# Kernel tuning notes

Hardware: AMD Instinct MI355X
Metric: run time of the kernel (lower is better)

The kernel has to match this reference:

```python
import jax, jax.numpy as jnp
import numpy as np

PAD = 1  # module padding

def setup_inputs() -> dict:
    key = jax.random.key(0)
    k1, k2 = jax.random.split(key)
    x = jax.random.normal(k1, (1, 256, 512, 512), dtype=jnp.float32)
    # module uses uniform(-xavier, xavier) with xavier = 1/sqrt(kh*kw)
    xavier = 1.0 / np.sqrt(3 * 3)
    weight = jax.random.uniform(k2, (256, 256, 3, 3), dtype=jnp.float32,
                                minval=-xavier, maxval=xavier)
    return {"x": x, "weight": weight}

def reference(x, weight):
    # Stride-1 cross-correlation with zero padding PAD, matching the
    # module's per-pixel slice*kernel sum (batch must be 1 for that code).
    return jax.lax.conv_general_dilated(
        x, weight,
        window_strides=(1, 1),
        padding=[(PAD, PAD), (PAD, PAD)],
        dimension_numbers=("NCHW", "OIHW", "NCHW"),
    )
```

## Files before the change

kernel.cpp:

```cpp
#include <hip/hip_runtime.h>
#include <stdint.h>

typedef __attribute__((ext_vector_type(8))) __bf16 bf16x8;
typedef __attribute__((ext_vector_type(16))) float f32x16;

constexpr int CIN = 256, COUT = 256, HH = 512, WW = 512;
constexpr int BC = 16;
constexpr int NCB = CIN / BC;
constexpr int CPAD = 20;
constexpr int MT = 128;
constexpr int TY = 8, TX = 32;

__device__ __forceinline__ unsigned short f2bf(float f) {
    union { float f; unsigned int u; } v; v.f = f;
    return (unsigned short)((v.u + 0x7fffu + ((v.u >> 16) & 1u)) >> 16);
}

__device__ __forceinline__ bf16x8 ldsfrag(const unsigned short* p) {
    union { unsigned long long u[2]; bf16x8 v; } r;
    r.u[0] = *reinterpret_cast<const unsigned long long*>(p);
    r.u[1] = *reinterpret_cast<const unsigned long long*>(p + 4);
    return r.v;
}

__global__ void wt_transform2(const float* __restrict__ w, unsigned short* __restrict__ wt2) {
    const int cbtap = blockIdx.x;
    const int cb = cbtap / 9, tap = cbtap - cb * 9;
    #pragma unroll 4
    for (int e = threadIdx.x; e < 4096; e += 256) {
        const int k = e >> 4, ci = e & 15;
        wt2[cbtap * 4096 + e] = f2bf(w[(k * CIN + cb * BC + ci) * 9 + tap]);
    }
}

__global__ __launch_bounds__(256)
void x_transform(const float* __restrict__ x, unsigned short* __restrict__ xb) {
    __shared__ unsigned short Xl[64][264];
    const int y  = blockIdx.x >> 3;
    const int x0 = (blockIdx.x & 7) * 64;
    #pragma unroll
    for (int q = threadIdx.x; q < 4096; q += 256) {
        const int c = q >> 4, p4 = (q & 15) << 2;
        const float4 v = *reinterpret_cast<const float4*>(
            x + ((long long)c * HH + y) * WW + x0 + p4);
        Xl[p4 + 0][c] = f2bf(v.x);
        Xl[p4 + 1][c] = f2bf(v.y);
        Xl[p4 + 2][c] = f2bf(v.z);
        Xl[p4 + 3][c] = f2bf(v.w);
    }
    __syncthreads();
    #pragma unroll
    for (int q = threadIdx.x; q < 2048; q += 256) {
        const int cb = q >> 7, rem = q & 127, px = rem >> 1, h = rem & 1;
        const int4 v = *reinterpret_cast<const int4*>(&Xl[px][cb * 16 + h * 8]);
        *reinterpret_cast<int4*>(
            xb + (((long long)cb * HH + y) * WW + x0 + px) * 16 + h * 8) = v;
    }
}

__global__ __launch_bounds__(256, 2)
void conv_mfma2(const unsigned short* __restrict__ xb, const unsigned short* __restrict__ wt2,
                float* __restrict__ out) {
    __shared__ unsigned short Wlds[9][MT][CPAD];
    __shared__ unsigned short Xt[TY + 2][TX + 2][CPAD];

    const int bid = blockIdx.x;
    const int k0 = (bid & 1) * MT;
    const int tile = bid >> 1;
    const int x0 = (tile & 15) * TX;
    const int y0 = (tile >> 4) * TY;

    const int tid = threadIdx.x;
    const int lane = tid & 63;
    const int wave = tid >> 6;
    const int wm = wave & 1;
    const int wn = wave >> 1;
    const int ln31 = lane & 31;
    const int lh8 = (lane >> 5) * 8;

    f32x16 acc[2][4];
    #pragma unroll
    for (int i = 0; i < 2; ++i)
        #pragma unroll
        for (int j = 0; j < 4; ++j)
            #pragma unroll
            for (int r = 0; r < 16; ++r) acc[i][j][r] = 0.f;

    for (int cb = 0; cb < NCB; ++cb) {
        #pragma unroll
        for (int e = tid; e < 9 * 256; e += 256) {
            const int tap = e >> 8;
            const int kk = (e >> 1) & 127;
            const int h = e & 1;
            const int4 v = *reinterpret_cast<const int4*>(
                wt2 + (((cb * 9 + tap) * 256 + k0 + kk) << 4) + h * 8);
            unsigned long long* d = reinterpret_cast<unsigned long long*>(&Wlds[tap][kk][h * 8]);
            const unsigned long long* s2 = reinterpret_cast<const unsigned long long*>(&v);
            d[0] = s2[0]; d[1] = s2[1];
        }

        for (int rr = wave; rr < TY + 2; rr += 4) {
            const int yy = y0 - 1 + rr;
            const bool rowok = ((unsigned)yy < (unsigned)HH);
            const int xi = lane >> 1, h = lane & 1;
            const int gx = x0 - 1 + xi;
            int4 v; v.x = v.y = v.z = v.w = 0;
            if (rowok && (unsigned)gx < (unsigned)WW)
                v = *reinterpret_cast<const int4*>(
                    xb + (((cb * HH + yy) * WW + gx) << 4) + h * 8);
            unsigned long long* d = reinterpret_cast<unsigned long long*>(&Xt[rr][xi][h * 8]);
            const unsigned long long* s2 = reinterpret_cast<const unsigned long long*>(&v);
            d[0] = s2[0]; d[1] = s2[1];
            if (lane < 4) {
                const int xi2 = 32 + (lane >> 1);
                const int gx2 = x0 - 1 + xi2;
                int4 v2; v2.x = v2.y = v2.z = v2.w = 0;
                if (rowok && gx2 < WW)
                    v2 = *reinterpret_cast<const int4*>(
                        xb + (((cb * HH + yy) * WW + gx2) << 4) + h * 8);
                unsigned long long* d2 = reinterpret_cast<unsigned long long*>(&Xt[rr][xi2][h * 8]);
                const unsigned long long* s3 = reinterpret_cast<const unsigned long long*>(&v2);
                d2[0] = s3[0]; d2[1] = s3[1];
            }
        }
        __syncthreads();

        #pragma unroll
        for (int rr = 0; rr < 3; ++rr) {
            #pragma unroll
            for (int s = 0; s < 3; ++s) {
                const int tap = rr * 3 + s;
                const bf16x8 a0 = ldsfrag(&Wlds[tap][wm * 64 + 0 + ln31][lh8]);
                const bf16x8 a1 = ldsfrag(&Wlds[tap][wm * 64 + 32 + ln31][lh8]);
                #pragma unroll
                for (int j = 0; j < 4; ++j) {
                    const bf16x8 b = ldsfrag(&Xt[wn * 4 + j + rr][s + ln31][lh8]);
                    acc[0][j] = __builtin_amdgcn_mfma_f32_32x32x16_bf16(a0, b, acc[0][j], 0, 0, 0);
                    acc[1][j] = __builtin_amdgcn_mfma_f32_32x32x16_bf16(a1, b, acc[1][j], 0, 0, 0);
                }
            }
        }
        __syncthreads();
    }

    #pragma unroll
    for (int i = 0; i < 2; ++i) {
        const int mb = k0 + wm * 64 + i * 32 + (lane >> 5) * 4;
        #pragma unroll
        for (int j = 0; j < 4; ++j) {
            const long long py = y0 + wn * 4 + j;
            const long long px = x0 + ln31;
            #pragma unroll
            for (int r = 0; r < 16; ++r) {
                const int m = mb + (r & 3) + 8 * (r >> 2);
                out[((long long)m * HH + py) * WW + px] = acc[i][j][r];
            }
        }
    }
}

__global__ void wt_transform(const float* __restrict__ w, unsigned short* __restrict__ wt) {
    int idx = blockIdx.x * 256 + threadIdx.x;
    int tap = idx >> 16;
    int rem = idx & 65535;
    int k = rem >> 8, c = rem & 255;
    wt[idx] = f2bf(w[((k << 8) | c) * 9 + tap]);
}

__global__ __launch_bounds__(256, 3)
void conv_mfma(const float* __restrict__ x, const unsigned short* __restrict__ wt,
               float* __restrict__ out) {
    __shared__ unsigned short Wlds[9][MT][CPAD];
    __shared__ unsigned short Xto[4 + 2][TX + 2][CPAD];

    const int bid = blockIdx.x;
    const int k0 = (bid & 1) * MT;
    const int tile = bid >> 1;
    const int x0 = (tile & 15) * TX;
    const int y0 = (tile >> 4) * 4;

    const int tid = threadIdx.x;
    const int lane = tid & 63;
    const int wave = tid >> 6;
    const int wm = wave & 1;
    const int wn = wave >> 1;
    const int ln31 = lane & 31;
    const int lh8 = (lane >> 5) * 8;

    f32x16 acc[2][2];
    #pragma unroll
    for (int i = 0; i < 2; ++i)
        #pragma unroll
        for (int j = 0; j < 2; ++j)
            #pragma unroll
            for (int r = 0; r < 16; ++r) acc[i][j][r] = 0.f;

    for (int cb = 0; cb < CIN / BC; ++cb) {
        const int c0 = cb * BC;
        for (int e = tid; e < 9 * MT; e += 256) {
            const int tap = e >> 7;
            const int k = e & (MT - 1);
            const unsigned long long* src = reinterpret_cast<const unsigned long long*>(
                wt + ((tap * COUT + (k0 + k)) * CIN + c0));
            unsigned long long* dst = reinterpret_cast<unsigned long long*>(&Wlds[tap][k][0]);
            dst[0] = src[0]; dst[1] = src[1]; dst[2] = src[2]; dst[3] = src[3];
        }
        {
            const int rowid = tid >> 5, lx = tid & 31;
            for (int p = rowid; p < 6 * BC; p += 8) {
                const int rr = p >> 4, c = p & 15;
                const int yy = y0 - 1 + rr;
                const bool rowok = ((unsigned)yy < (unsigned)HH);
                const float* xrow = x + (long long)(c0 + c) * (HH * WW) + (long long)yy * WW;
                const int gx = x0 - 1 + lx;
                float v0 = (rowok && (unsigned)gx < (unsigned)WW) ? xrow[gx] : 0.f;
                Xto[rr][lx][c] = f2bf(v0);
                if (lx < 2) {
                    const int gx2 = x0 + 31 + lx;
                    float v1 = (rowok && gx2 < WW) ? xrow[gx2] : 0.f;
                    Xto[rr][32 + lx][c] = f2bf(v1);
                }
            }
        }
        __syncthreads();
        #pragma unroll
        for (int rr = 0; rr < 3; ++rr) {
            #pragma unroll
            for (int s = 0; s < 3; ++s) {
                const int tap = rr * 3 + s;
                bf16x8 a0 = ldsfrag(&Wlds[tap][wm * 64 + 0 + ln31][lh8]);
                bf16x8 a1 = ldsfrag(&Wlds[tap][wm * 64 + 32 + ln31][lh8]);
                bf16x8 b0 = ldsfrag(&Xto[wn * 2 + 0 + rr][s + ln31][lh8]);
                bf16x8 b1 = ldsfrag(&Xto[wn * 2 + 1 + rr][s + ln31][lh8]);
                acc[0][0] = __builtin_amdgcn_mfma_f32_32x32x16_bf16(a0, b0, acc[0][0], 0, 0, 0);
                acc[0][1] = __builtin_amdgcn_mfma_f32_32x32x16_bf16(a0, b1, acc[0][1], 0, 0, 0);
                acc[1][0] = __builtin_amdgcn_mfma_f32_32x32x16_bf16(a1, b0, acc[1][0], 0, 0, 0);
                acc[1][1] = __builtin_amdgcn_mfma_f32_32x32x16_bf16(a1, b1, acc[1][1], 0, 0, 0);
            }
        }
        __syncthreads();
    }

    #pragma unroll
    for (int i = 0; i < 2; ++i) {
        const int mb = k0 + wm * 64 + i * 32 + (lane >> 5) * 4;
        #pragma unroll
        for (int j = 0; j < 2; ++j) {
            const long long py = y0 + wn * 2 + j;
            const long long px = x0 + ln31;
            #pragma unroll
            for (int r = 0; r < 16; ++r) {
                const int m = mb + (r & 3) + 8 * (r >> 2);
                out[((long long)m * HH + py) * WW + px] = acc[i][j][r];
            }
        }
    }
}

__global__ void conv_naive(const float* __restrict__ x, const float* __restrict__ w,
                           float* __restrict__ out) {
    const int k = blockIdx.x;
    const int y = blockIdx.y;
    const int xx = blockIdx.z * 256 + threadIdx.x;
    float a = 0.f;
    for (int c = 0; c < CIN; ++c) {
        const float* wp = w + ((k * CIN + c) * 9);
        const float* xp = x + (long long)c * HH * WW;
        #pragma unroll
        for (int r = 0; r < 3; ++r) {
            const int yy = y + r - 1;
            if ((unsigned)yy >= (unsigned)HH) continue;
            const float* row = xp + (long long)yy * WW;
            #pragma unroll
            for (int s = 0; s < 3; ++s) {
                const int gx = xx + s - 1;
                const float v = ((unsigned)gx < (unsigned)WW) ? row[gx] : 0.f;
                a += wp[r * 3 + s] * v;
            }
        }
    }
    out[((long long)k * HH + y) * WW + xx] = a;
}

extern "C" void kernel_launch(void* const* d_in, const int* in_sizes, int n_in,
                              void* d_out, int out_size, void* d_ws, size_t ws_size,
                              hipStream_t stream) {
    const float* x = (const float*)d_in[0];
    const float* w = (const float*)d_in[1];
    float* out = (float*)d_out;

    const size_t xb_bytes  = (size_t)NCB * HH * WW * BC * sizeof(unsigned short);
    const size_t wt2_bytes = (size_t)144 * 4096 * sizeof(unsigned short);
    const size_t wt_bytes  = (size_t)9 * 256 * 256 * sizeof(unsigned short);

    if (ws_size >= xb_bytes + wt2_bytes) {
        unsigned short* xb  = (unsigned short*)d_ws;
        unsigned short* wt2 = (unsigned short*)d_ws + xb_bytes / sizeof(unsigned short);
        x_transform<<<4096, 256, 0, stream>>>(x, xb);
        wt_transform2<<<144, 256, 0, stream>>>(w, wt2);
        conv_mfma2<<<2048, 256, 0, stream>>>(xb, wt2, out);
    } else if (ws_size >= wt_bytes) {
        unsigned short* wt = (unsigned short*)d_ws;
        wt_transform<<<2304, 256, 0, stream>>>(w, wt);
        conv_mfma<<<4096, 256, 0, stream>>>(x, wt, out);
    } else {
        conv_naive<<<dim3(256, 512, 2), 256, 0, stream>>>(x, w, out);
    }
}
```

Before: 792.4 us.

## Load conv tiles via global_load_lds, drop LDS padding, swizzle blocks, retile x_transform

Replaces the register-staged global-to-LDS copies in the main conv kernel with direct global_load_lds transfers into unpadded 16-element-wide LDS tiles. Out-of-bounds halo pixels are read from a zeroed global buffer. The next channel block's loads are now issued right after the compute with explicit waitcnt and barriers, and block IDs are swizzled so blocks sharing a tile land near each other. It also splits x_transform into smaller per-channel-group blocks and removes the mid-size fallback path. The risk is that dropping the padding brings back LDS bank conflicts on the bf16x8 fragment reads, and loads are still not double-buffered.

```diff
diff --git a/kernel.cpp b/kernel.cpp
--- a/kernel.cpp
+++ b/kernel.cpp
@@ -7,7 +7,6 @@
 constexpr int CIN = 256, COUT = 256, HH = 512, WW = 512;
 constexpr int BC = 16;
 constexpr int NCB = CIN / BC;
-constexpr int CPAD = 20;
 constexpr int MT = 128;
 constexpr int TY = 8, TX = 32;
 
@@ -16,11 +15,12 @@
     return (unsigned short)((v.u + 0x7fffu + ((v.u >> 16) & 1u)) >> 16);
 }
 
-__device__ __forceinline__ bf16x8 ldsfrag(const unsigned short* p) {
-    union { unsigned long long u[2]; bf16x8 v; } r;
-    r.u[0] = *reinterpret_cast<const unsigned long long*>(p);
-    r.u[1] = *reinterpret_cast<const unsigned long long*>(p + 4);
-    return r.v;
+__device__ __align__(256) unsigned short g_zero16[16] = {};
+
+__device__ __forceinline__ void gload16(const void* g, const void* l) {
+    __builtin_amdgcn_global_load_lds(
+        (const __attribute__((address_space(1))) unsigned int*)g,
+        (__attribute__((address_space(3))) unsigned int*)l, 16, 0, 0);
 }
 
 __global__ void wt_transform2(const float* __restrict__ w, unsigned short* __restrict__ wt2) {
@@ -35,38 +35,43 @@
 
 __global__ __launch_bounds__(256)
 void x_transform(const float* __restrict__ x, unsigned short* __restrict__ xb) {
-    __shared__ unsigned short Xl[64][264];
-    const int y  = blockIdx.x >> 3;
-    const int x0 = (blockIdx.x & 7) * 64;
-    #pragma unroll
-    for (int q = threadIdx.x; q < 4096; q += 256) {
-        const int c = q >> 4, p4 = (q & 15) << 2;
+    __shared__ __align__(16) float Xl[16][72];
+    const int b   = blockIdx.x;
+    const int y   = b >> 5;
+    const int xc  = (b >> 2) & 7;
+    const int cbg = b & 3;
+    const int x0  = xc * 64;
+    const int tid = threadIdx.x;
+    const int ci  = tid >> 4, p4 = (tid & 15) << 2;
+    const int px  = tid >> 2, cig = tid & 3;
+    #pragma unroll 1
+    for (int g = 0; g < 4; ++g) {
+        const int cb = cbg * 4 + g;
         const float4 v = *reinterpret_cast<const float4*>(
-            x + ((long long)c * HH + y) * WW + x0 + p4);
-        Xl[p4 + 0][c] = f2bf(v.x);
-        Xl[p4 + 1][c] = f2bf(v.y);
-        Xl[p4 + 2][c] = f2bf(v.z);
-        Xl[p4 + 3][c] = f2bf(v.w);
-    }
-    __syncthreads();
-    #pragma unroll
-    for (int q = threadIdx.x; q < 2048; q += 256) {
-        const int cb = q >> 7, rem = q & 127, px = rem >> 1, h = rem & 1;
-        const int4 v = *reinterpret_cast<const int4*>(&Xl[px][cb * 16 + h * 8]);
-        *reinterpret_cast<int4*>(
-            xb + (((long long)cb * HH + y) * WW + x0 + px) * 16 + h * 8) = v;
+            x + ((long long)(cb * 16 + ci) * HH + y) * WW + x0 + p4);
+        *reinterpret_cast<float4*>(&Xl[ci][p4]) = v;
+        __syncthreads();
+        ushort4 o;
+        o.x = f2bf(Xl[cig * 4 + 0][px]);
+        o.y = f2bf(Xl[cig * 4 + 1][px]);
+        o.z = f2bf(Xl[cig * 4 + 2][px]);
+        o.w = f2bf(Xl[cig * 4 + 3][px]);
+        *reinterpret_cast<ushort4*>(
+            xb + (((long long)cb * HH + y) * WW + x0 + px) * 16 + cig * 4) = o;
+        __syncthreads();
     }
 }
 
 __global__ __launch_bounds__(256, 2)
-void conv_mfma2(const unsigned short* __restrict__ xb, const unsigned short* __restrict__ wt2,
+void conv_mfma3(const unsigned short* __restrict__ xb, const unsigned short* __restrict__ wt2,
                 float* __restrict__ out) {
-    __shared__ unsigned short Wlds[9][MT][CPAD];
-    __shared__ unsigned short Xt[TY + 2][TX + 2][CPAD];
+    __shared__ __align__(16) unsigned short Wl[9][MT][16];
+    __shared__ __align__(16) unsigned short Xs[TY + 2][36][16];
 
     const int bid = blockIdx.x;
-    const int k0 = (bid & 1) * MT;
-    const int tile = bid >> 1;
+    const int swz = ((bid & 7) << 8) | (bid >> 3);
+    const int k0 = (swz & 1) * MT;
+    const int tile = swz >> 1;
     const int x0 = (tile & 15) * TX;
     const int y0 = (tile >> 4) * TY;
 
@@ -86,61 +91,84 @@
             #pragma unroll
             for (int r = 0; r < 16; ++r) acc[i][j][r] = 0.f;
 
+    const unsigned short* wsrc0 = wt2 + (size_t)k0 * 16 + (size_t)tid * 8;
+    unsigned short* wl = ((unsigned short*)Wl) + (tid >> 6) * 512;
+
+    {
+        const unsigned short* wsrc = wsrc0;
+        #pragma unroll
+        for (int i = 0; i < 9; ++i)
+            gload16(wsrc + (size_t)i * 4096, wl + i * 2048);
+        #pragma unroll
+        for (int t = 0; t < 3; ++t) {
+            const int rr = wave + t * 4;
+            if (rr < TY + 2) {
+                const int yy = y0 - 1 + rr;
+                const bool rok = (unsigned)yy < (unsigned)HH;
+                const size_t rowb = ((size_t)0 * HH + (rok ? yy : 0)) * WW;
+                const int gx = x0 - 1 + (lane >> 1);
+                const bool ok = rok && ((unsigned)gx < (unsigned)WW);
+                const unsigned short* gs = ok ? xb + (rowb + gx) * 16 + (lane & 1) * 8 : g_zero16;
+                gload16(gs, &Xs[rr][0][0]);
+                if (lane < 8) {
+                    const int gx2 = x0 + 31 + (lane >> 1);
+                    const bool ok2 = rok && gx2 < WW;
+                    const unsigned short* gs2 = ok2 ? xb + (rowb + gx2) * 16 + (lane & 1) * 8 : g_zero16;
+                    gload16(gs2, &Xs[rr][32][0]);
+                }
+            }
+        }
+        asm volatile("s_waitcnt vmcnt(0)" ::: "memory");
+        __builtin_amdgcn_s_barrier();
+    }
+
     for (int cb = 0; cb < NCB; ++cb) {
         #pragma unroll
-        for (int e = tid; e < 9 * 256; e += 256) {
-            const int tap = e >> 8;
-            const int kk = (e >> 1) & 127;
-            const int h = e & 1;
-            const int4 v = *reinterpret_cast<const int4*>(
-                wt2 + (((cb * 9 + tap) * 256 + k0 + kk) << 4) + h * 8);
-            unsigned long long* d = reinterpret_cast<unsigned long long*>(&Wlds[tap][kk][h * 8]);
-            const unsigned long long* s2 = reinterpret_cast<const unsigned long long*>(&v);
-            d[0] = s2[0]; d[1] = s2[1];
-        }
-
-        for (int rr = wave; rr < TY + 2; rr += 4) {
-            const int yy = y0 - 1 + rr;
-            const bool rowok = ((unsigned)yy < (unsigned)HH);
-            const int xi = lane >> 1, h = lane & 1;
-            const int gx = x0 - 1 + xi;
-            int4 v; v.x = v.y = v.z = v.w = 0;
-            if (rowok && (unsigned)gx < (unsigned)WW)
-                v = *reinterpret_cast<const int4*>(
-                    xb + (((cb * HH + yy) * WW + gx) << 4) + h * 8);
-            unsigned long long* d = reinterpret_cast<unsigned long long*>(&Xt[rr][xi][h * 8]);
-            const unsigned long long* s2 = reinterpret_cast<const unsigned long long*>(&v);
-            d[0] = s2[0]; d[1] = s2[1];
-            if (lane < 4) {
-                const int xi2 = 32 + (lane >> 1);
-                const int gx2 = x0 - 1 + xi2;
-                int4 v2; v2.x = v2.y = v2.z = v2.w = 0;
-                if (rowok && gx2 < WW)
-                    v2 = *reinterpret_cast<const int4*>(
-                        xb + (((cb * HH + yy) * WW + gx2) << 4) + h * 8);
-                unsigned long long* d2 = reinterpret_cast<unsigned long long*>(&Xt[rr][xi2][h * 8]);
-                const unsigned long long* s3 = reinterpret_cast<const unsigned long long*>(&v2);
-                d2[0] = s3[0]; d2[1] = s3[1];
-            }
-        }
-        __syncthreads();
-
-        #pragma unroll
-        for (int rr = 0; rr < 3; ++rr) {
-            #pragma unroll
-            for (int s = 0; s < 3; ++s) {
+        for (int s = 0; s < 3; ++s) {
+            #pragma unroll
+            for (int rr = 0; rr < 3; ++rr) {
                 const int tap = rr * 3 + s;
-                const bf16x8 a0 = ldsfrag(&Wlds[tap][wm * 64 + 0 + ln31][lh8]);
-                const bf16x8 a1 = ldsfrag(&Wlds[tap][wm * 64 + 32 + ln31][lh8]);
+                const bf16x8 a0 = *reinterpret_cast<const bf16x8*>(&Wl[tap][wm * 64 + ln31][lh8]);
+                const bf16x8 a1 = *reinterpret_cast<const bf16x8*>(&Wl[tap][wm * 64 + 32 + ln31][lh8]);
                 #pragma unroll
                 for (int j = 0; j < 4; ++j) {
-                    const bf16x8 b = ldsfrag(&Xt[wn * 4 + j + rr][s + ln31][lh8]);
+                    const bf16x8 b = *reinterpret_cast<const bf16x8*>(&Xs[wn * 4 + j + rr][s + ln31][lh8]);
                     acc[0][j] = __builtin_amdgcn_mfma_f32_32x32x16_bf16(a0, b, acc[0][j], 0, 0, 0);
                     acc[1][j] = __builtin_amdgcn_mfma_f32_32x32x16_bf16(a1, b, acc[1][j], 0, 0, 0);
                 }
             }
         }
-        __syncthreads();
+
+        if (cb + 1 < NCB) {
+            const int cn = cb + 1;
+            asm volatile("s_waitcnt lgkmcnt(0)" ::: "memory");
+            __builtin_amdgcn_s_barrier();
+            const unsigned short* wsrc = wsrc0 + (size_t)cn * 9 * 4096;
+            #pragma unroll
+            for (int i = 0; i < 9; ++i)
+                gload16(wsrc + (size_t)i * 4096, wl + i * 2048);
+            #pragma unroll
+            for (int t = 0; t < 3; ++t) {
+                const int rr = wave + t * 4;
+                if (rr < TY + 2) {
+                    const int yy = y0 - 1 + rr;
+                    const bool rok = (unsigned)yy < (unsigned)HH;
+                    const size_t rowb = ((size_t)cn * HH + (rok ? yy : 0)) * WW;
+                    const int gx = x0 - 1 + (lane >> 1);
+                    const bool ok = rok && ((unsigned)gx < (unsigned)WW);
+                    const unsigned short* gs = ok ? xb + (rowb + gx) * 16 + (lane & 1) * 8 : g_zero16;
+                    gload16(gs, &Xs[rr][0][0]);
+                    if (lane < 8) {
+                        const int gx2 = x0 + 31 + (lane >> 1);
+                        const bool ok2 = rok && gx2 < WW;
+                        const unsigned short* gs2 = ok2 ? xb + (rowb + gx2) * 16 + (lane & 1) * 8 : g_zero16;
+                        gload16(gs2, &Xs[rr][32][0]);
+                    }
+                }
+            }
+            asm volatile("s_waitcnt vmcnt(0)" ::: "memory");
+            __builtin_amdgcn_s_barrier();
+        }
     }
 
     #pragma unroll
@@ -149,104 +177,6 @@
         #pragma unroll
         for (int j = 0; j < 4; ++j) {
             const long long py = y0 + wn * 4 + j;
-            const long long px = x0 + ln31;
-            #pragma unroll
-            for (int r = 0; r < 16; ++r) {
-                const int m = mb + (r & 3) + 8 * (r >> 2);
-                out[((long long)m * HH + py) * WW + px] = acc[i][j][r];
-            }
-        }
-    }
-}
-
-__global__ void wt_transform(const float* __restrict__ w, unsigned short* __restrict__ wt) {
-    int idx = blockIdx.x * 256 + threadIdx.x;
-    int tap = idx >> 16;
-    int rem = idx & 65535;
-    int k = rem >> 8, c = rem & 255;
-    wt[idx] = f2bf(w[((k << 8) | c) * 9 + tap]);
-}
-
-__global__ __launch_bounds__(256, 3)
-void conv_mfma(const float* __restrict__ x, const unsigned short* __restrict__ wt,
-               float* __restrict__ out) {
-    __shared__ unsigned short Wlds[9][MT][CPAD];
-    __shared__ unsigned short Xto[4 + 2][TX + 2][CPAD];
-
-    const int bid = blockIdx.x;
-    const int k0 = (bid & 1) * MT;
-    const int tile = bid >> 1;
-    const int x0 = (tile & 15) * TX;
-    const int y0 = (tile >> 4) * 4;
-
-    const int tid = threadIdx.x;
-    const int lane = tid & 63;
-    const int wave = tid >> 6;
-    const int wm = wave & 1;
-    const int wn = wave >> 1;
-    const int ln31 = lane & 31;
-    const int lh8 = (lane >> 5) * 8;
-
-    f32x16 acc[2][2];
-    #pragma unroll
-    for (int i = 0; i < 2; ++i)
-        #pragma unroll
-        for (int j = 0; j < 2; ++j)
-            #pragma unroll
-            for (int r = 0; r < 16; ++r) acc[i][j][r] = 0.f;
-
-    for (int cb = 0; cb < CIN / BC; ++cb) {
-        const int c0 = cb * BC;
-        for (int e = tid; e < 9 * MT; e += 256) {
-            const int tap = e >> 7;
-            const int k = e & (MT - 1);
-            const unsigned long long* src = reinterpret_cast<const unsigned long long*>(
-                wt + ((tap * COUT + (k0 + k)) * CIN + c0));
-            unsigned long long* dst = reinterpret_cast<unsigned long long*>(&Wlds[tap][k][0]);
-            dst[0] = src[0]; dst[1] = src[1]; dst[2] = src[2]; dst[3] = src[3];
-        }
-        {
-            const int rowid = tid >> 5, lx = tid & 31;
-            for (int p = rowid; p < 6 * BC; p += 8) {
-                const int rr = p >> 4, c = p & 15;
-                const int yy = y0 - 1 + rr;
-                const bool rowok = ((unsigned)yy < (unsigned)HH);
-                const float* xrow = x + (long long)(c0 + c) * (HH * WW) + (long long)yy * WW;
-                const int gx = x0 - 1 + lx;
-                float v0 = (rowok && (unsigned)gx < (unsigned)WW) ? xrow[gx] : 0.f;
-                Xto[rr][lx][c] = f2bf(v0);
-                if (lx < 2) {
-                    const int gx2 = x0 + 31 + lx;
-                    float v1 = (rowok && gx2 < WW) ? xrow[gx2] : 0.f;
-                    Xto[rr][32 + lx][c] = f2bf(v1);
-                }
-            }
-        }
-        __syncthreads();
-        #pragma unroll
-        for (int rr = 0; rr < 3; ++rr) {
-            #pragma unroll
-            for (int s = 0; s < 3; ++s) {
-                const int tap = rr * 3 + s;
-                bf16x8 a0 = ldsfrag(&Wlds[tap][wm * 64 + 0 + ln31][lh8]);
-                bf16x8 a1 = ldsfrag(&Wlds[tap][wm * 64 + 32 + ln31][lh8]);
-                bf16x8 b0 = ldsfrag(&Xto[wn * 2 + 0 + rr][s + ln31][lh8]);
-                bf16x8 b1 = ldsfrag(&Xto[wn * 2 + 1 + rr][s + ln31][lh8]);
-                acc[0][0] = __builtin_amdgcn_mfma_f32_32x32x16_bf16(a0, b0, acc[0][0], 0, 0, 0);
-                acc[0][1] = __builtin_amdgcn_mfma_f32_32x32x16_bf16(a0, b1, acc[0][1], 0, 0, 0);
-                acc[1][0] = __builtin_amdgcn_mfma_f32_32x32x16_bf16(a1, b0, acc[1][0], 0, 0, 0);
-                acc[1][1] = __builtin_amdgcn_mfma_f32_32x32x16_bf16(a1, b1, acc[1][1], 0, 0, 0);
-            }
-        }
-        __syncthreads();
-    }
-
-    #pragma unroll
-    for (int i = 0; i < 2; ++i) {
-        const int mb = k0 + wm * 64 + i * 32 + (lane >> 5) * 4;
-        #pragma unroll
-        for (int j = 0; j < 2; ++j) {
-            const long long py = y0 + wn * 2 + j;
             const long long px = x0 + ln31;
             #pragma unroll
             for (int r = 0; r < 16; ++r) {
@@ -291,18 +221,13 @@
 
     const size_t xb_bytes  = (size_t)NCB * HH * WW * BC * sizeof(unsigned short);
     const size_t wt2_bytes = (size_t)144 * 4096 * sizeof(unsigned short);
-    const size_t wt_bytes  = (size_t)9 * 256 * 256 * sizeof(unsigned short);
 
     if (ws_size >= xb_bytes + wt2_bytes) {
         unsigned short* xb  = (unsigned short*)d_ws;
         unsigned short* wt2 = (unsigned short*)d_ws + xb_bytes / sizeof(unsigned short);
-        x_transform<<<4096, 256, 0, stream>>>(x, xb);
+        x_transform<<<16384, 256, 0, stream>>>(x, xb);
         wt_transform2<<<144, 256, 0, stream>>>(w, wt2);
-        conv_mfma2<<<2048, 256, 0, stream>>>(xb, wt2, out);
-    } else if (ws_size >= wt_bytes) {
-        unsigned short* wt = (unsigned short*)d_ws;
-        wt_transform<<<2304, 256, 0, stream>>>(w, wt);
-        conv_mfma<<<4096, 256, 0, stream>>>(x, wt, out);
+        conv_mfma3<<<2048, 256, 0, stream>>>(xb, wt2, out);
     } else {
         conv_naive<<<dim3(256, 512, 2), 256, 0, stream>>>(x, w, out);
     }
```

Measured after the change: 692.3 us. 12.6% less time.
